# Kernel tuning notes

Hardware: AMD Instinct MI355X
Metric: run time of the kernel (lower is better)

Reference implementation:

```python
import jax, jax.numpy as jnp
import numpy as np

B, A, FEAT = 16, 256, 64
HID = 256
TEMB = 32
NUM_T = 100
L = 4
E = 131072
N = B * A


def _remove_mean(x):
    # x: [B, A, 3]
    return x - jnp.mean(x, axis=1, keepdims=True)


def setup_inputs() -> dict:
    key = jax.random.key(0)
    ks = jax.random.split(key, 24)
    s = 0.02
    inp = {
        "h": jax.random.normal(ks[0], (B, A, FEAT), jnp.float32),
        "x0": jax.random.normal(ks[1], (B, A, 3), jnp.float32),
        "noise": jax.random.normal(ks[2], (B, A, 3), jnp.float32),
        "t": jax.random.randint(ks[3], (B,), 0, NUM_T, jnp.int32),
        "row": jax.random.randint(ks[4], (E,), 0, N, jnp.int32),
        "col": jax.random.randint(ks[5], (E,), 0, N, jnp.int32),
        # node embedding
        "W_emb": jax.random.normal(ks[6], (FEAT + TEMB, HID), jnp.float32) * s,
        "b_emb": jnp.zeros((HID,), jnp.float32),
        # per-layer EGNN params, stacked over L layers
        "eW1": jax.random.normal(ks[7], (L, 2 * HID + 1, HID), jnp.float32) * s,
        "eb1": jnp.zeros((L, HID), jnp.float32),
        "eW2": jax.random.normal(ks[8], (L, HID, HID), jnp.float32) * s,
        "eb2": jnp.zeros((L, HID), jnp.float32),
        "cW1": jax.random.normal(ks[9], (L, HID, HID), jnp.float32) * s,
        "cb1": jnp.zeros((L, HID), jnp.float32),
        "cW2": jax.random.normal(ks[10], (L, HID, 1), jnp.float32) * s,
        "nW1": jax.random.normal(ks[11], (L, 2 * HID, HID), jnp.float32) * s,
        "nb1": jnp.zeros((L, HID), jnp.float32),
        "nW2": jax.random.normal(ks[12], (L, HID, HID), jnp.float32) * s,
        "nb2": jnp.zeros((L, HID), jnp.float32),
    }
    return inp


def _time_embedding(t):
    half = TEMB // 2
    freq = jnp.exp(jnp.arange(half, dtype=jnp.float32) * (-np.log(10000.0) / (half - 1)))
    ang = t.astype(jnp.float32)[:, None] * freq[None, :]  # [B, half]
    return jnp.concatenate([jnp.sin(ang), jnp.cos(ang)], axis=-1)  # [B, TEMB]


def _egnn_layer(h, x, row, col, eW1, eb1, eW2, eb2, cW1, cb1, cW2, nW1, nb1, nW2, nb2):
    coord_diff = x[row] - x[col]                                  # [E, 3]
    radial = jnp.sum(coord_diff * coord_diff, axis=1, keepdims=True)  # [E, 1]
    edge_in = jnp.concatenate([h[row], h[col], radial], axis=1)   # [E, 2H+1]
    m = jax.nn.silu(edge_in @ eW1 + eb1)
    m_ij = jax.nn.silu(m @ eW2 + eb2)                             # [E, H]
    w = jax.nn.silu(m_ij @ cW1 + cb1) @ cW2                       # [E, 1]
    coord_update = coord_diff * w                                 # [E, 3]
    x_new = x + jax.ops.segment_sum(coord_update, row, num_segments=N)
    m_i = jax.ops.segment_sum(m_ij, row, num_segments=N)          # [N, H]
    node_in = jnp.concatenate([h, m_i], axis=1)
    h_new = h + (jax.nn.silu(node_in @ nW1 + nb1) @ nW2 + nb2)
    return h_new, x_new


def reference(h, x0, noise, W_emb, b_emb, eW1, eb1, eW2, eb2, cW1, cb1, cW2,
              nW1, nb1, nW2, nb2, t, row, col):
    # diffusion schedule
    betas = jnp.linspace(1e-4, 0.02, NUM_T, dtype=jnp.float32)
    alphas_cumprod = jnp.cumprod(1.0 - betas)
    # forward diffusion q(x_t | x_0)
    noise = _remove_mean(noise)
    ab = alphas_cumprod[t][:, None, None]                          # [B,1,1]
    xt = jnp.sqrt(ab) * x0 + jnp.sqrt(1.0 - ab) * noise
    xt = _remove_mean(xt)

    t_emb = _time_embedding(t)                                     # [B, TEMB]
    t_emb_flat = jnp.repeat(t_emb, A, axis=0)                      # [N, TEMB]
    h_flat = h.reshape(N, FEAT)
    xt_flat = xt.reshape(N, 3)
    h_in = jnp.concatenate([h_flat, t_emb_flat], axis=-1)

    hh = h_in @ W_emb + b_emb                                      # [N, H]
    xx = xt_flat
    for l in range(L):
        hh, xx = _egnn_layer(hh, xx, row, col,
                             eW1[l], eb1[l], eW2[l], eb2[l],
                             cW1[l], cb1[l], cW2[l],
                             nW1[l], nb1[l], nW2[l], nb2[l])

    noise_pred = (xx - xt_flat).reshape(B, A, 3)
    noise_pred = _remove_mean(noise_pred)
    loss = jnp.mean((noise_pred - noise) ** 2)
    return loss
```

## Files before the change

### kernel.cpp

```cpp
#include <hip/hip_runtime.h>

#define NB 16
#define NA 256
#define NNODES 4096
#define FEATD 64
#define HID 256
#define TEMBD 32
#define NUMT 100
#define NE 131072
#define NL 4
#define NCHUNK (NE / 16)

typedef __attribute__((ext_vector_type(8))) short short8;
typedef __attribute__((ext_vector_type(4))) float f32x4;
typedef __attribute__((ext_vector_type(2))) float f32x2;

__device__ __forceinline__ float silu_f(float v) {
    float s = __builtin_amdgcn_rcpf(1.f + __builtin_amdgcn_exp2f(-1.44269504f * v));
    return v * s;
}

__device__ __forceinline__ short f2bf(float f) {
    union { float f; unsigned u; } v; v.f = f;
    unsigned r = (v.u + 0x7fffu + ((v.u >> 16) & 1u)) >> 16;
    return (short)r;
}
__device__ __forceinline__ short f2bf_t(float f) {
    union { float f; unsigned u; } v; v.f = f;
    return (short)(v.u >> 16);
}
__device__ __forceinline__ float bf2f(short s) {
    union { float f; unsigned u; } v; v.u = ((unsigned)(unsigned short)s) << 16;
    return v.f;
}

__device__ __forceinline__ float block_sum(float v, float* red, int a) {
    red[a] = v; __syncthreads();
    for (int s = 128; s > 0; s >>= 1) {
        if (a < s) red[a] += red[a + s];
        __syncthreads();
    }
    float r = red[0]; __syncthreads();
    return r;
}

__global__ __launch_bounds__(256) void prep_kernel(
    const float* __restrict__ x0, const float* __restrict__ noise,
    const int* __restrict__ t,
    float* __restrict__ noise_c, float* __restrict__ xt, float* __restrict__ temb,
    int* __restrict__ deg, float* __restrict__ out)
{
    __shared__ float red[256];
    __shared__ float sab_s[2];
    int b = blockIdx.x, a = threadIdx.x;
    int base = (b * NA + a) * 3;

    deg[b * 256 + a] = 0;
    if (b == 0 && a == 0) out[0] = 0.f;

    float nx = noise[base + 0], ny = noise[base + 1], nz = noise[base + 2];
    float mnx = block_sum(nx, red, a) * (1.f / NA);
    float mny = block_sum(ny, red, a) * (1.f / NA);
    float mnz = block_sum(nz, red, a) * (1.f / NA);
    nx -= mnx; ny -= mny; nz -= mnz;
    noise_c[base + 0] = nx; noise_c[base + 1] = ny; noise_c[base + 2] = nz;

    if (a == 0) {
        int tt = t[b];
        float p = 1.f;
        for (int i = 0; i < NUMT; i++) {
            float beta = 1e-4f + (0.02f - 1e-4f) * (float)i / (float)(NUMT - 1);
            if (i <= tt) p *= (1.f - beta);
        }
        sab_s[0] = sqrtf(p);
        sab_s[1] = sqrtf(1.f - p);
    }
    __syncthreads();
    float sab = sab_s[0], s1ab = sab_s[1];

    float xx = sab * x0[base + 0] + s1ab * nx;
    float xy = sab * x0[base + 1] + s1ab * ny;
    float xz = sab * x0[base + 2] + s1ab * nz;
    float mx = block_sum(xx, red, a) * (1.f / NA);
    float my = block_sum(xy, red, a) * (1.f / NA);
    float mz = block_sum(xz, red, a) * (1.f / NA);
    xt[base + 0] = xx - mx; xt[base + 1] = xy - my; xt[base + 2] = xz - mz;

    if (a < TEMBD / 2) {
        float fr = expf(-logf(10000.f) * (float)a / (float)(TEMBD / 2 - 1));
        float ang = (float)t[b] * fr;
        temb[b * TEMBD + a] = sinf(ang);
        temb[b * TEMBD + TEMBD / 2 + a] = cosf(ang);
    }
}

__global__ __launch_bounds__(256) void csr_hist(const int* __restrict__ row, int* __restrict__ deg)
{
    int i = blockIdx.x * 256 + threadIdx.x;
    if (i < NE) atomicAdd(&deg[row[i]], 1);
}

__global__ __launch_bounds__(256) void csr_scan(const int* __restrict__ deg, int* __restrict__ cursor)
{
    __shared__ int s[256];
    int t = threadIdx.x;
    int base = t * 16;
    int loc[16];
    int sum = 0;
    for (int i = 0; i < 16; i++) { loc[i] = sum; sum += deg[base + i]; }
    s[t] = sum; __syncthreads();
    for (int off = 1; off < 256; off <<= 1) {
        int v = (t >= off) ? s[t - off] : 0;
        __syncthreads();
        s[t] += v;
        __syncthreads();
    }
    int excl = (t == 0) ? 0 : s[t - 1];
    for (int i = 0; i < 16; i++) cursor[base + i] = excl + loc[i];
}

__global__ __launch_bounds__(256) void csr_scatter(
    const int* __restrict__ row, const int* __restrict__ col,
    int* __restrict__ cursor, int* __restrict__ prow, int* __restrict__ pcol)
{
    int i = blockIdx.x * 256 + threadIdx.x;
    if (i < NE) {
        int r = row[i];
        int p = atomicAdd(&cursor[r], 1);
        prow[p] = r;
        pcol[p] = col[i];
    }
}

__global__ __launch_bounds__(256) void csr_flag(
    const int* __restrict__ cursor, int* __restrict__ flag)
{
    int r = blockIdx.x * 256 + threadIdx.x;
    if (r >= NNODES) return;
    int end = cursor[r];
    int start = (r == 0) ? 0 : cursor[r - 1];
    int fl = 0;
    if (end > start) {
        int cs = start >> 4, ce = (end - 1) >> 4;
        for (int ch = cs; ch <= ce; ch++) {
            int rs = start > ch * 16 ? start : ch * 16;
            int re = end < ch * 16 + 16 ? end : ch * 16 + 16;
            if (rs > ch * 16 && re < ch * 16 + 16) fl = 1;
        }
    }
    flag[r] = fl;
}

#define WOFF_EMB 0
#define WOFF_L(l) (24576 + (l) * 458752)
#define WOFF_AB 0
#define WOFF_E2 131072
#define WOFF_C1 196608
#define WOFF_N1 262144
#define WOFF_N2 393216
#define W_TOTAL (24576 + 4 * 458752)

__global__ __launch_bounds__(256) void convert_weights(
    const float* __restrict__ W_emb, const float* __restrict__ eW1,
    const float* __restrict__ eW2, const float* __restrict__ cW1,
    const float* __restrict__ nW1, const float* __restrict__ nW2,
    short* __restrict__ wb)
{
    int idx = blockIdx.x * 256 + threadIdx.x;
    if (idx >= W_TOTAL) return;
    if (idx < 24576) {
        int k = idx >> 8, n = idx & 255;
        wb[WOFF_EMB + ((k >> 5) << 13) + (n << 5) + (k & 31)] = f2bf(W_emb[idx]);
        return;
    }
    int r = idx - 24576;
    int l = r / 458752;
    int o = r - l * 458752;
    if (o < 131072) {
        int k = o >> 9, n = o & 511;
        const float* src = eW1 + (size_t)l * 513 * 256 +
            (n < 256 ? (size_t)k * 256 + n : (size_t)(256 + k) * 256 + (n - 256));
        wb[WOFF_L(l) + WOFF_AB + ((k >> 5) * 16384) + (n << 5) + (k & 31)] = f2bf(*src);
        return;
    }
    const float* src; int dst; int o2;
    if (o < 196608)      { o2 = o - 131072; src = eW2 + (size_t)l * 65536 + o2;  dst = WOFF_L(l) + WOFF_E2; }
    else if (o < 262144) { o2 = o - 196608; src = cW1 + (size_t)l * 65536 + o2;  dst = WOFF_L(l) + WOFF_C1; }
    else if (o < 393216) { o2 = o - 262144; src = nW1 + (size_t)l * 131072 + o2; dst = WOFF_L(l) + WOFF_N1; }
    else                 { o2 = o - 393216; src = nW2 + (size_t)l * 65536 + o2;  dst = WOFF_L(l) + WOFF_N2; }
    int k = o2 >> 8, n = o2 & 255;
    wb[dst + ((k >> 5) << 13) + (n << 5) + (k & 31)] = f2bf(*src);
}

#define WF8_TOTAL (4 * 2 * 65536)
__global__ __launch_bounds__(256) void convert_weights_fp8(
    const float* __restrict__ eW2, const float* __restrict__ cW1,
    char* __restrict__ wf8)
{
    int idx = blockIdx.x * 256 + threadIdx.x;
    if (idx >= WF8_TOTAL) return;
    int l = idx >> 17;
    int o = idx & 131071;
    int mat = o >> 16;
    int o2 = o & 65535;
    int k = o2 >> 8, n = o2 & 255;
    const float* src = (mat == 0 ? eW2 : cW1) + (size_t)l * 65536 + (size_t)k * 256 + n;
    float v = (*src) * 16.f;
    int p = __builtin_amdgcn_cvt_pk_fp8_f32(v, v, 0, false);
    wf8[(size_t)l * 131072 + mat * 65536 + (k >> 5) * 8192 + n * 32 + (k & 31)] = (char)(p & 0xff);
}

__global__ __launch_bounds__(1024) void emb_p12_fused(
    const float* __restrict__ h, const float* __restrict__ temb,
    const short* __restrict__ wtEmb,
    const float* __restrict__ b_emb, const short* __restrict__ wtAB,
    const float* __restrict__ eb1_0,
    short* __restrict__ hh, short* __restrict__ P12)
{
    __shared__ short h2s[16 * 264];
    int tid = threadIdx.x;
    int wv = tid >> 6, l = tid & 63;
    int lr = l & 15, q = l >> 4;
    int r0 = blockIdx.x * 16;

    f32x4 acc = (f32x4){0.f, 0.f, 0.f, 0.f};
    int col0 = wv * 16 + lr;
    int n = r0 + lr;
    #pragma unroll
    for (int kt = 0; kt < 3; kt++) {
        int kk = kt * 32 + q * 8;
        const float* src = (kk < 64) ? &h[(size_t)n * 64 + kk]
                                     : &temb[(n >> 8) * 32 + kk - 64];
        short8 fa;
        #pragma unroll
        for (int k2 = 0; k2 < 8; k2++) fa[k2] = f2bf(src[k2]);
        short8 fb = *(const short8*)&wtEmb[kt * 8192 + col0 * 32 + q * 8];
        acc = __builtin_amdgcn_mfma_f32_16x16x32_bf16(fa, fb, acc, 0, 0, 0);
    }
    {
        float bv = b_emb[col0];
        #pragma unroll
        for (int rg = 0; rg < 4; rg++) {
            int rrow = q * 4 + rg;
            short b = f2bf(acc[rg] + bv);
            hh[(size_t)(r0 + rrow) * 256 + col0] = b;
            h2s[rrow * 264 + col0] = b;
        }
    }
    __syncthreads();

    f32x4 acc3[2];
    #pragma unroll
    for (int i = 0; i < 2; i++) acc3[i] = (f32x4){0.f, 0.f, 0.f, 0.f};
    #pragma unroll 2
    for (int kt = 0; kt < 8; kt++) {
        short8 fa = *(const short8*)&h2s[lr * 264 + kt * 32 + q * 8];
        #pragma unroll
        for (int nt = 0; nt < 2; nt++) {
            short8 fb = *(const short8*)&wtAB[kt * 16384 + (wv * 32 + nt * 16 + lr) * 32 + q * 8];
            acc3[nt] = __builtin_amdgcn_mfma_f32_16x16x32_bf16(fa, fb, acc3[nt], 0, 0, 0);
        }
    }
    #pragma unroll
    for (int nt = 0; nt < 2; nt++) {
        int col = wv * 32 + nt * 16 + lr;
        float bv = (col < 256) ? eb1_0[col] : 0.f;
        #pragma unroll
        for (int rg = 0; rg < 4; rg++)
            P12[(size_t)(r0 + q * 4 + rg) * 512 + col] = f2bf(acc3[nt][rg] + bv);
    }
}

__global__ __launch_bounds__(1024) void node_p12_fused(
    const short* __restrict__ hc, const float* __restrict__ m_i,
    const int* __restrict__ cursor, const int* __restrict__ flag,
    const int* __restrict__ tag0, const int* __restrict__ tag1,
    const float* __restrict__ msl0, const float* __restrict__ msl1,
    const float* __restrict__ xsl0, const float* __restrict__ xsl1,
    const float* __restrict__ x_agg, float* __restrict__ x_cur,
    const short* __restrict__ wtN1, const float* __restrict__ nb1,
    const short* __restrict__ wtN2, const float* __restrict__ nb2,
    const short* __restrict__ wtAB, const float* __restrict__ eb1n,
    short* __restrict__ hn, short* __restrict__ P12)
{
    __shared__ short m_is[16 * 264];
    __shared__ short t1s[16 * 264];
    __shared__ short h2s[16 * 264];
    int tid = threadIdx.x;
    int wv = tid >> 6, l = tid & 63;
    int lr = l & 15, q = l >> 4;
    int r0 = blockIdx.x * 16;

    {
        int rr = tid >> 6;
        int cc = (tid & 63) * 4;
        int r = r0 + rr;
        float v[4] = {0.f, 0.f, 0.f, 0.f};
        if (flag[r]) {
            float4 mv = *(const float4*)&m_i[(size_t)r * 256 + cc];
            v[0] = mv.x; v[1] = mv.y; v[2] = mv.z; v[3] = mv.w;
        }
        int end = cursor[r];
        int start = (r == 0) ? 0 : cursor[r - 1];
        if (end > start) {
            int cs = start >> 4, ce = (end - 1) >> 4;
            for (int ch = cs; ch <= ce; ch++) {
                if (tag0[ch] == r) {
                    float4 s0 = *(const float4*)&msl0[(size_t)ch * 256 + cc];
                    v[0] += s0.x; v[1] += s0.y; v[2] += s0.z; v[3] += s0.w;
                }
                if (tag1[ch] == r) {
                    float4 s1 = *(const float4*)&msl1[(size_t)ch * 256 + cc];
                    v[0] += s1.x; v[1] += s1.y; v[2] += s1.z; v[3] += s1.w;
                }
            }
        }
        #pragma unroll
        for (int i = 0; i < 4; i++) m_is[rr * 264 + cc + i] = f2bf(v[i]);
        if (tid < 16) {
            int r2 = r0 + tid;
            float sx = 0.f, sy = 0.f, sz = 0.f;
            if (flag[r2]) {
                sx = x_agg[r2 * 3 + 0]; sy = x_agg[r2 * 3 + 1]; sz = x_agg[r2 * 3 + 2];
            }
            int end2 = cursor[r2];
            int start2 = (r2 == 0) ? 0 : cursor[r2 - 1];
            if (end2 > start2) {
                int cs2 = start2 >> 4, ce2 = (end2 - 1) >> 4;
                for (int ch = cs2; ch <= ce2; ch++) {
                    if (tag0[ch] == r2) { sx += xsl0[ch * 3 + 0]; sy += xsl0[ch * 3 + 1]; sz += xsl0[ch * 3 + 2]; }
                    if (tag1[ch] == r2) { sx += xsl1[ch * 3 + 0]; sy += xsl1[ch * 3 + 1]; sz += xsl1[ch * 3 + 2]; }
                }
            }
            x_cur[r2 * 3 + 0] += sx;
            x_cur[r2 * 3 + 1] += sy;
            x_cur[r2 * 3 + 2] += sz;
        }
    }
    __syncthreads();

    int col0 = wv * 16 + lr;
    f32x4 acc = (f32x4){0.f, 0.f, 0.f, 0.f};
    #pragma unroll 2
    for (int kt = 0; kt < 16; kt++) {
        int kk = kt * 32 + q * 8;
        short8 fa;
        if (kk < 256) fa = *(const short8*)&hc[(size_t)(r0 + lr) * 256 + kk];
        else          fa = *(const short8*)&m_is[lr * 264 + kk - 256];
        short8 fb = *(const short8*)&wtN1[kt * 8192 + col0 * 32 + q * 8];
        acc = __builtin_amdgcn_mfma_f32_16x16x32_bf16(fa, fb, acc, 0, 0, 0);
    }
    {
        float bv = nb1[col0];
        #pragma unroll
        for (int rg = 0; rg < 4; rg++)
            t1s[(q * 4 + rg) * 264 + col0] = f2bf_t(silu_f(acc[rg] + bv));
    }
    __syncthreads();

    f32x4 acc2 = (f32x4){0.f, 0.f, 0.f, 0.f};
    #pragma unroll 2
    for (int kt = 0; kt < 8; kt++) {
        short8 fa = *(const short8*)&t1s[lr * 264 + kt * 32 + q * 8];
        short8 fb = *(const short8*)&wtN2[kt * 8192 + col0 * 32 + q * 8];
        acc2 = __builtin_amdgcn_mfma_f32_16x16x32_bf16(fa, fb, acc2, 0, 0, 0);
    }
    {
        float bv = nb2[col0];
        #pragma unroll
        for (int rg = 0; rg < 4; rg++) {
            int rrow = q * 4 + rg;
            float v = acc2[rg] + bv + bf2f(hc[(size_t)(r0 + rrow) * 256 + col0]);
            short b = f2bf(v);
            hn[(size_t)(r0 + rrow) * 256 + col0] = b;
            h2s[rrow * 264 + col0] = b;
        }
    }
    __syncthreads();

    f32x4 acc3[2];
    #pragma unroll
    for (int i = 0; i < 2; i++) acc3[i] = (f32x4){0.f, 0.f, 0.f, 0.f};
    #pragma unroll 2
    for (int kt = 0; kt < 8; kt++) {
        short8 fa = *(const short8*)&h2s[lr * 264 + kt * 32 + q * 8];
        #pragma unroll
        for (int nt = 0; nt < 2; nt++) {
            short8 fb = *(const short8*)&wtAB[kt * 16384 + (wv * 32 + nt * 16 + lr) * 32 + q * 8];
            acc3[nt] = __builtin_amdgcn_mfma_f32_16x16x32_bf16(fa, fb, acc3[nt], 0, 0, 0);
        }
    }
    #pragma unroll
    for (int nt = 0; nt < 2; nt++) {
        int col = wv * 32 + nt * 16 + lr;
        float bv = (col < 256) ? eb1n[col] : 0.f;
        #pragma unroll
        for (int rg = 0; rg < 4; rg++)
            P12[(size_t)(r0 + q * 4 + rg) * 512 + col] = f2bf(acc3[nt][rg] + bv);
    }
}

__global__ __launch_bounds__(256, 4) void egnn_edge_mfma(
    const short* __restrict__ P12, const float* __restrict__ x,
    const int* __restrict__ prow, const int* __restrict__ pcol,
    const float* __restrict__ w512,
    const char* __restrict__ wf8E2, const float* __restrict__ eb2,
    const char* __restrict__ wf8C1, const float* __restrict__ cb1,
    const float* __restrict__ cW2,
    float* __restrict__ m_i, float* __restrict__ x_agg,
    float* __restrict__ msl0, float* __restrict__ msl1,
    float* __restrict__ xsl0, float* __restrict__ xsl1,
    int* __restrict__ tag0, int* __restrict__ tag1, int do_mi)
{
    __shared__ __align__(16) char m_lds[64 * 272];
    __shared__ float cd_s[64][3];
    __shared__ int prow_s[64];
    __shared__ float wred[4][64];
    __shared__ float xtmp[64][3];

    int tid = threadIdx.x;
    int e0 = blockIdx.x * 64;
    int wv = tid >> 6, l = tid & 63;
    int lr = l & 15, q = l >> 4;

    {
        int e = tid >> 2, cq = tid & 3;
        int r = prow[e0 + e], c = pcol[e0 + e];
        float dx = x[r * 3 + 0] - x[c * 3 + 0];
        float dy = x[r * 3 + 1] - x[c * 3 + 1];
        float dz = x[r * 3 + 2] - x[c * 3 + 2];
        float rad = dx * dx + dy * dy + dz * dz;
        if (cq == 0) {
            prow_s[e] = r;
            cd_s[e][0] = dx; cd_s[e][1] = dy; cd_s[e][2] = dz;
        }
        const short* p1r = P12 + (size_t)r * 512;
        const short* p2r = P12 + (size_t)c * 512 + 256;
        #pragma unroll
        for (int j = 0; j < 8; j++) {
            int cb = (j >> 1) * 64 + (j & 1) * 32 + cq * 8;
            short8 a = *(const short8*)&p1r[cb];
            short8 b = *(const short8*)&p2r[cb];
            float4 w0 = *(const float4*)&w512[cb];
            float4 w1 = *(const float4*)&w512[cb + 4];
            float wv8[8] = {w0.x, w0.y, w0.z, w0.w, w1.x, w1.y, w1.z, w1.w};
            float s[8];
            #pragma unroll
            for (int k2 = 0; k2 < 8; k2++)
                s[k2] = silu_f(bf2f(a[k2]) + bf2f(b[k2]) + rad * wv8[k2]);
            int lo = __builtin_amdgcn_cvt_pk_fp8_f32(s[0], s[1], 0, false);
            lo = __builtin_amdgcn_cvt_pk_fp8_f32(s[2], s[3], lo, true);
            int hi = __builtin_amdgcn_cvt_pk_fp8_f32(s[4], s[5], 0, false);
            hi = __builtin_amdgcn_cvt_pk_fp8_f32(s[6], s[7], hi, true);
            int2 d = {lo, hi};
            *(int2*)&m_lds[e * 272 + cb] = d;
        }
    }
    __syncthreads();

    f32x4 acc[4][4];
    #pragma unroll
    for (int i = 0; i < 4; i++)
        #pragma unroll
        for (int j = 0; j < 4; j++) acc[i][j] = (f32x4){0.f, 0.f, 0.f, 0.f};
    #pragma unroll 2
    for (int kt = 0; kt < 8; kt++) {
        long fa[4], fb[4];
        #pragma unroll
        for (int mt = 0; mt < 4; mt++)
            fa[mt] = *(const long*)&m_lds[(mt * 16 + lr) * 272 + kt * 32 + q * 8];
        #pragma unroll
        for (int nt = 0; nt < 4; nt++)
            fb[nt] = *(const long*)&wf8E2[kt * 8192 + (wv * 64 + nt * 16 + lr) * 32 + q * 8];
        #pragma unroll
        for (int mt = 0; mt < 4; mt++)
            #pragma unroll
            for (int nt = 0; nt < 4; nt++)
                acc[mt][nt] = __builtin_amdgcn_mfma_f32_16x16x32_fp8_fp8(fa[mt], fb[nt], acc[mt][nt], 0, 0, 0);
    }
    __syncthreads();
    #pragma unroll
    for (int nt = 0; nt < 4; nt++) {
        int ccol = wv * 64 + nt * 16 + lr;
        float b2 = eb2[ccol];
        #pragma unroll
        for (int mt = 0; mt < 4; mt++)
            #pragma unroll
            for (int rg = 0; rg < 4; rg++) {
                int e = mt * 16 + q * 4 + rg;
                float v = silu_f(fmaf(acc[mt][nt][rg], 0.0625f, b2));
                int p = __builtin_amdgcn_cvt_pk_fp8_f32(v, v, 0, false);
                m_lds[e * 272 + ccol] = (char)(p & 0xff);
            }
    }
    __syncthreads();

    #pragma unroll
    for (int i = 0; i < 4; i++)
        #pragma unroll
        for (int j = 0; j < 4; j++) acc[i][j] = (f32x4){0.f, 0.f, 0.f, 0.f};
    #pragma unroll 2
    for (int kt = 0; kt < 8; kt++) {
        long fa[4], fb[4];
        #pragma unroll
        for (int mt = 0; mt < 4; mt++)
            fa[mt] = *(const long*)&m_lds[(mt * 16 + lr) * 272 + kt * 32 + q * 8];
        #pragma unroll
        for (int nt = 0; nt < 4; nt++)
            fb[nt] = *(const long*)&wf8C1[kt * 8192 + (wv * 64 + nt * 16 + lr) * 32 + q * 8];
        #pragma unroll
        for (int mt = 0; mt < 4; mt++)
            #pragma unroll
            for (int nt = 0; nt < 4; nt++)
                acc[mt][nt] = __builtin_amdgcn_mfma_f32_16x16x32_fp8_fp8(fa[mt], fb[nt], acc[mt][nt], 0, 0, 0);
    }

    if (do_mi) {
        int ebase = wv * 16;
        int c4 = l * 4;
        int chunk = blockIdx.x * 4 + wv;
        float a0 = 0.f, a1 = 0.f, a2 = 0.f, a3 = 0.f;
        int cur = prow_s[ebase];
        int nrun = 0;
        #pragma unroll
        for (int j = 0; j < 16; j++) {
            int e = ebase + j;
            int r = prow_s[e];
            if (r != cur) {
                float4 v = {a0, a1, a2, a3};
                if (nrun == 0) *(float4*)&msl0[(size_t)chunk * 256 + c4] = v;
                else           *(float4*)&m_i[(size_t)cur * 256 + c4] = v;
                nrun++; a0 = a1 = a2 = a3 = 0.f; cur = r;
            }
            int mv = *(const int*)&m_lds[e * 272 + c4];
            f32x2 lo = __builtin_amdgcn_cvt_pk_f32_fp8(mv, false);
            f32x2 hi = __builtin_amdgcn_cvt_pk_f32_fp8(mv, true);
            a0 += lo.x; a1 += lo.y; a2 += hi.x; a3 += hi.y;
        }
        float4 v = {a0, a1, a2, a3};
        if (nrun == 0) *(float4*)&msl0[(size_t)chunk * 256 + c4] = v;
        else           *(float4*)&msl1[(size_t)chunk * 256 + c4] = v;
        if (l == 0) {
            tag0[chunk] = prow_s[ebase];
            tag1[chunk] = nrun ? cur : -1;
        }
    }

    {
        float wp[4][4];
        #pragma unroll
        for (int i = 0; i < 4; i++)
            #pragma unroll
            for (int j = 0; j < 4; j++) wp[i][j] = 0.f;
        #pragma unroll
        for (int nt = 0; nt < 4; nt++) {
            int ccol = wv * 64 + nt * 16 + lr;
            float b1 = cb1[ccol];
            float c2 = cW2[ccol];
            #pragma unroll
            for (int mt = 0; mt < 4; mt++)
                #pragma unroll
                for (int rg = 0; rg < 4; rg++)
                    wp[mt][rg] += silu_f(fmaf(acc[mt][nt][rg], 0.0625f, b1)) * c2;
        }
        #pragma unroll
        for (int mt = 0; mt < 4; mt++)
            #pragma unroll
            for (int rg = 0; rg < 4; rg++) {
                float v = wp[mt][rg];
                v += __shfl_xor(v, 1, 64);
                v += __shfl_xor(v, 2, 64);
                v += __shfl_xor(v, 4, 64);
                v += __shfl_xor(v, 8, 64);
                if (lr == 0) wred[wv][mt * 16 + q * 4 + rg] = v;
            }
    }
    __syncthreads();
    if (tid < 64) {
        float w = wred[0][tid] + wred[1][tid] + wred[2][tid] + wred[3][tid];
        xtmp[tid][0] = cd_s[tid][0] * w;
        xtmp[tid][1] = cd_s[tid][1] * w;
        xtmp[tid][2] = cd_s[tid][2] * w;
    }
    __syncthreads();
    if (tid < 64) {
        int e = tid, j = e & 15, cw = e >> 4;
        int r = prow_s[e];
        bool leader = (j == 0) || (prow_s[e - 1] != r);
        if (leader) {
            int eend = (cw + 1) * 16;
            float sx = 0.f, sy = 0.f, sz = 0.f;
            int k = e;
            while (k < eend && prow_s[k] == r) {
                sx += xtmp[k][0]; sy += xtmp[k][1]; sz += xtmp[k][2]; k++;
            }
            int chunk = blockIdx.x * 4 + cw;
            if (j == 0)        { xsl0[chunk * 3 + 0] = sx; xsl0[chunk * 3 + 1] = sy; xsl0[chunk * 3 + 2] = sz; }
            else if (k == eend){ xsl1[chunk * 3 + 0] = sx; xsl1[chunk * 3 + 1] = sy; xsl1[chunk * 3 + 2] = sz; }
            else               { x_agg[r * 3 + 0] = sx; x_agg[r * 3 + 1] = sy; x_agg[r * 3 + 2] = sz; }
        }
    }
}

__global__ __launch_bounds__(256) void loss_part(
    const float* __restrict__ x_cur, const float* __restrict__ xt,
    const float* __restrict__ nc,
    const int* __restrict__ cursor, const int* __restrict__ flag,
    const int* __restrict__ tag0, const int* __restrict__ tag1,
    const float* __restrict__ xsl0, const float* __restrict__ xsl1,
    const float* __restrict__ x_agg,
    float* __restrict__ out)
{
    __shared__ float red[256];
    int b = blockIdx.x, a = threadIdx.x;
    int n = b * NA + a;
    int base = n * 3;

    float sx = 0.f, sy = 0.f, sz = 0.f;
    if (flag[n]) {
        sx = x_agg[base + 0]; sy = x_agg[base + 1]; sz = x_agg[base + 2];
    }
    int end = cursor[n];
    int start = (n == 0) ? 0 : cursor[n - 1];
    if (end > start) {
        int cs = start >> 4, ce = (end - 1) >> 4;
        for (int ch = cs; ch <= ce; ch++) {
            if (tag0[ch] == n) { sx += xsl0[ch * 3 + 0]; sy += xsl0[ch * 3 + 1]; sz += xsl0[ch * 3 + 2]; }
            if (tag1[ch] == n) { sx += xsl1[ch * 3 + 0]; sy += xsl1[ch * 3 + 1]; sz += xsl1[ch * 3 + 2]; }
        }
    }
    float px = x_cur[base + 0] + sx - xt[base + 0];
    float py = x_cur[base + 1] + sy - xt[base + 1];
    float pz = x_cur[base + 2] + sz - xt[base + 2];
    float mx = block_sum(px, red, a) * (1.f / NA);
    float my = block_sum(py, red, a) * (1.f / NA);
    float mz = block_sum(pz, red, a) * (1.f / NA);
    px -= mx; py -= my; pz -= mz;
    float dx = px - nc[base + 0], dy = py - nc[base + 1], dz = pz - nc[base + 2];
    float s = block_sum(dx * dx + dy * dy + dz * dz, red, a);
    if (a == 0) atomicAdd(out, s * (1.f / (float)(NNODES * 3)));
}

extern "C" void kernel_launch(void* const* d_in, const int* in_sizes, int n_in,
                              void* d_out, int out_size, void* d_ws, size_t ws_size,
                              hipStream_t stream)
{
    (void)in_sizes; (void)n_in; (void)out_size; (void)ws_size;
    const float* h     = (const float*)d_in[0];
    const float* x0    = (const float*)d_in[1];
    const float* noise = (const float*)d_in[2];
    const int*   t     = (const int*)d_in[3];
    const int*   row   = (const int*)d_in[4];
    const int*   col   = (const int*)d_in[5];
    const float* W_emb = (const float*)d_in[6];
    const float* b_emb = (const float*)d_in[7];
    const float* eW1   = (const float*)d_in[8];
    const float* eb1   = (const float*)d_in[9];
    const float* eW2   = (const float*)d_in[10];
    const float* eb2   = (const float*)d_in[11];
    const float* cW1   = (const float*)d_in[12];
    const float* cb1   = (const float*)d_in[13];
    const float* cW2   = (const float*)d_in[14];
    const float* nW1   = (const float*)d_in[15];
    const float* nb1   = (const float*)d_in[16];
    const float* nW2   = (const float*)d_in[17];
    const float* nb2   = (const float*)d_in[18];

    float* f = (float*)d_ws;
    size_t fo = 0;
    float* temb    = f + fo; fo += NB * TEMBD;
    float* noise_c = f + fo; fo += NNODES * 3;
    float* xt      = f + fo; fo += NNODES * 3;
    float* x_cur   = f + fo; fo += NNODES * 3;
    float* x_agg   = f + fo; fo += NNODES * 3;
    float* m_i     = f + fo; fo += (size_t)NNODES * HID;
    float* msl0    = f + fo; fo += (size_t)NCHUNK * 256;
    float* msl1    = f + fo; fo += (size_t)NCHUNK * 256;
    float* xsl0    = f + fo; fo += (size_t)NCHUNK * 3;
    float* xsl1    = f + fo; fo += (size_t)NCHUNK * 3;

    int* iw = (int*)(f + fo);
    size_t io = 0;
    int* deg    = iw + io; io += NNODES;
    int* cursor = iw + io; io += NNODES;
    int* flag   = iw + io; io += NNODES;
    int* prow   = iw + io; io += NE;
    int* pcol   = iw + io; io += NE;
    int* tag0   = iw + io; io += NCHUNK;
    int* tag1   = iw + io; io += NCHUNK;

    size_t sbase_bytes = ((((char*)(iw + io)) - (char*)d_ws) + 15) & ~(size_t)15;
    short* sb = (short*)((char*)d_ws + sbase_bytes);
    short* wb  = sb;
    size_t so = W_TOTAL;
    short* hh  = sb + so; so += (size_t)NNODES * HID;
    short* hh2 = sb + so; so += (size_t)NNODES * HID;
    short* P12 = sb + so; so += (size_t)NNODES * 512;
    char* wf8 = (char*)(sb + so);

    prep_kernel<<<NB, 256, 0, stream>>>(x0, noise, t, noise_c, xt, temb, deg, (float*)d_out);
    csr_hist<<<NE / 256, 256, 0, stream>>>(row, deg);
    csr_scan<<<1, 256, 0, stream>>>(deg, cursor);
    csr_scatter<<<NE / 256, 256, 0, stream>>>(row, col, cursor, prow, pcol);
    csr_flag<<<NNODES / 256, 256, 0, stream>>>(cursor, flag);
    convert_weights<<<(W_TOTAL + 255) / 256, 256, 0, stream>>>(W_emb, eW1, eW2, cW1, nW1, nW2, wb);
    convert_weights_fp8<<<WF8_TOTAL / 256, 256, 0, stream>>>(eW2, cW1, wf8);
    emb_p12_fused<<<NNODES / 16, 1024, 0, stream>>>(
        h, temb, wb + WOFF_EMB, b_emb, wb + WOFF_L(0) + WOFF_AB, eb1, hh, P12);
    hipMemcpyAsync(x_cur, xt, (size_t)NNODES * 3 * sizeof(float), hipMemcpyDeviceToDevice, stream);

    short* hc = hh;
    short* hn = hh2;
    for (int l = 0; l < NL; l++) {
        const short* wl = wb + WOFF_L(l);
        const char* wf8l = wf8 + (size_t)l * 131072;
        int last = (l == NL - 1);
        egnn_edge_mfma<<<NE / 64, 256, 0, stream>>>(
            P12, x_cur, prow, pcol,
            eW1 + (size_t)l * 513 * 256 + 512 * 256,
            wf8l, eb2 + (size_t)l * HID,
            wf8l + 65536, cb1 + (size_t)l * HID,
            cW2 + (size_t)l * HID,
            m_i, x_agg, msl0, msl1, xsl0, xsl1, tag0, tag1, last ? 0 : 1);
        if (!last) {
            node_p12_fused<<<NNODES / 16, 1024, 0, stream>>>(
                hc, m_i, cursor, flag, tag0, tag1, msl0, msl1,
                xsl0, xsl1, x_agg, x_cur,
                wl + WOFF_N1, nb1 + (size_t)l * HID,
                wl + WOFF_N2, nb2 + (size_t)l * HID,
                wb + WOFF_L(l + 1) + WOFF_AB, eb1 + (size_t)(l + 1) * HID,
                hn, P12);
            short* tmp = hc; hc = hn; hn = tmp;
        }
    }

    loss_part<<<NB, 256, 0, stream>>>(
        x_cur, xt, noise_c, cursor, flag, tag0, tag1, xsl0, xsl1, x_agg, (float*)d_out);
}
```

Measured before the change: 440.5 us.

## Fold small setup kernels together and retile node GEMMs to eight-row blocks

Three small launches disappear: the per-node flag computation moves into the CSR scan kernel, the fp8 weight conversion merges into the bf16 weight conversion, and the prep kernel writes x_cur directly instead of a device-to-device copy. The embedding and node-update fused kernels now use 8-row blocks of 512 threads, each wave covering more output columns. This doubles the grid for better CU coverage, but half of each 16-row MFMA tile holds duplicated rows, so matrix work per useful row doubles.

After: 468.3 us. 1.06x slower.

```diff
diff --git a/kernel.cpp b/kernel.cpp
--- a/kernel.cpp
+++ b/kernel.cpp
@@ -48,7 +48,7 @@
     const float* __restrict__ x0, const float* __restrict__ noise,
     const int* __restrict__ t,
     float* __restrict__ noise_c, float* __restrict__ xt, float* __restrict__ temb,
-    int* __restrict__ deg, float* __restrict__ out)
+    int* __restrict__ deg, float* __restrict__ out, float* __restrict__ x_cur)
 {
     __shared__ float red[256];
     __shared__ float sab_s[2];
@@ -84,7 +84,9 @@
     float mx = block_sum(xx, red, a) * (1.f / NA);
     float my = block_sum(xy, red, a) * (1.f / NA);
     float mz = block_sum(xz, red, a) * (1.f / NA);
-    xt[base + 0] = xx - mx; xt[base + 1] = xy - my; xt[base + 2] = xz - mz;
+    float vx = xx - mx, vy = xy - my, vz = xz - mz;
+    xt[base + 0] = vx; xt[base + 1] = vy; xt[base + 2] = vz;
+    x_cur[base + 0] = vx; x_cur[base + 1] = vy; x_cur[base + 2] = vz;
 
     if (a < TEMBD / 2) {
         float fr = expf(-logf(10000.f) * (float)a / (float)(TEMBD / 2 - 1));
@@ -100,14 +102,15 @@
     if (i < NE) atomicAdd(&deg[row[i]], 1);
 }
 
-__global__ __launch_bounds__(256) void csr_scan(const int* __restrict__ deg, int* __restrict__ cursor)
+__global__ __launch_bounds__(256) void csr_scan(
+    const int* __restrict__ deg, int* __restrict__ cursor, int* __restrict__ flag)
 {
     __shared__ int s[256];
     int t = threadIdx.x;
     int base = t * 16;
-    int loc[16];
+    int loc[16], dg[16];
     int sum = 0;
-    for (int i = 0; i < 16; i++) { loc[i] = sum; sum += deg[base + i]; }
+    for (int i = 0; i < 16; i++) { dg[i] = deg[base + i]; loc[i] = sum; sum += dg[i]; }
     s[t] = sum; __syncthreads();
     for (int off = 1; off < 256; off <<= 1) {
         int v = (t >= off) ? s[t - off] : 0;
@@ -116,7 +119,21 @@
         __syncthreads();
     }
     int excl = (t == 0) ? 0 : s[t - 1];
-    for (int i = 0; i < 16; i++) cursor[base + i] = excl + loc[i];
+    for (int i = 0; i < 16; i++) {
+        int start = excl + loc[i];
+        cursor[base + i] = start;
+        int end = start + dg[i];
+        int fl = 0;
+        if (end > start) {
+            int cs = start >> 4, ce = (end - 1) >> 4;
+            for (int ch = cs; ch <= ce; ch++) {
+                int rs = start > ch * 16 ? start : ch * 16;
+                int re = end < ch * 16 + 16 ? end : ch * 16 + 16;
+                if (rs > ch * 16 && re < ch * 16 + 16) fl = 1;
+            }
+        }
+        flag[base + i] = fl;
+    }
 }
 
 __global__ __launch_bounds__(256) void csr_scatter(
@@ -130,25 +147,6 @@
         prow[p] = r;
         pcol[p] = col[i];
     }
-}
-
-__global__ __launch_bounds__(256) void csr_flag(
-    const int* __restrict__ cursor, int* __restrict__ flag)
-{
-    int r = blockIdx.x * 256 + threadIdx.x;
-    if (r >= NNODES) return;
-    int end = cursor[r];
-    int start = (r == 0) ? 0 : cursor[r - 1];
-    int fl = 0;
-    if (end > start) {
-        int cs = start >> 4, ce = (end - 1) >> 4;
-        for (int ch = cs; ch <= ce; ch++) {
-            int rs = start > ch * 16 ? start : ch * 16;
-            int re = end < ch * 16 + 16 ? end : ch * 16 + 16;
-            if (rs > ch * 16 && re < ch * 16 + 16) fl = 1;
-        }
-    }
-    flag[r] = fl;
 }
 
 #define WOFF_EMB 0
@@ -159,15 +157,29 @@
 #define WOFF_N1 262144
 #define WOFF_N2 393216
 #define W_TOTAL (24576 + 4 * 458752)
+#define WF8_TOTAL (4 * 2 * 65536)
 
 __global__ __launch_bounds__(256) void convert_weights(
     const float* __restrict__ W_emb, const float* __restrict__ eW1,
     const float* __restrict__ eW2, const float* __restrict__ cW1,
     const float* __restrict__ nW1, const float* __restrict__ nW2,
-    short* __restrict__ wb)
+    short* __restrict__ wb, char* __restrict__ wf8)
 {
     int idx = blockIdx.x * 256 + threadIdx.x;
-    if (idx >= W_TOTAL) return;
+    if (idx >= W_TOTAL) {
+        int i8 = idx - W_TOTAL;
+        if (i8 >= WF8_TOTAL) return;
+        int l = i8 >> 17;
+        int o = i8 & 131071;
+        int mat = o >> 16;
+        int o2 = o & 65535;
+        int k = o2 >> 8, n = o2 & 255;
+        const float* src = (mat == 0 ? eW2 : cW1) + (size_t)l * 65536 + (size_t)k * 256 + n;
+        float v = (*src) * 16.f;
+        int p = __builtin_amdgcn_cvt_pk_fp8_f32(v, v, 0, false);
+        wf8[(size_t)l * 131072 + mat * 65536 + (k >> 5) * 8192 + n * 32 + (k & 31)] = (char)(p & 0xff);
+        return;
+    }
     if (idx < 24576) {
         int k = idx >> 8, n = idx & 255;
         wb[WOFF_EMB + ((k >> 5) << 13) + (n << 5) + (k & 31)] = f2bf(W_emb[idx]);
@@ -192,40 +204,24 @@
     wb[dst + ((k >> 5) << 13) + (n << 5) + (k & 31)] = f2bf(*src);
 }
 
-#define WF8_TOTAL (4 * 2 * 65536)
-__global__ __launch_bounds__(256) void convert_weights_fp8(
-    const float* __restrict__ eW2, const float* __restrict__ cW1,
-    char* __restrict__ wf8)
-{
-    int idx = blockIdx.x * 256 + threadIdx.x;
-    if (idx >= WF8_TOTAL) return;
-    int l = idx >> 17;
-    int o = idx & 131071;
-    int mat = o >> 16;
-    int o2 = o & 65535;
-    int k = o2 >> 8, n = o2 & 255;
-    const float* src = (mat == 0 ? eW2 : cW1) + (size_t)l * 65536 + (size_t)k * 256 + n;
-    float v = (*src) * 16.f;
-    int p = __builtin_amdgcn_cvt_pk_fp8_f32(v, v, 0, false);
-    wf8[(size_t)l * 131072 + mat * 65536 + (k >> 5) * 8192 + n * 32 + (k & 31)] = (char)(p & 0xff);
-}
-
-__global__ __launch_bounds__(1024) void emb_p12_fused(
+__global__ __launch_bounds__(512, 4) void emb_p12_fused(
     const float* __restrict__ h, const float* __restrict__ temb,
     const short* __restrict__ wtEmb,
     const float* __restrict__ b_emb, const short* __restrict__ wtAB,
     const float* __restrict__ eb1_0,
     short* __restrict__ hh, short* __restrict__ P12)
 {
-    __shared__ short h2s[16 * 264];
+    __shared__ short h2s[8 * 264];
     int tid = threadIdx.x;
     int wv = tid >> 6, l = tid & 63;
     int lr = l & 15, q = l >> 4;
-    int r0 = blockIdx.x * 16;
-
-    f32x4 acc = (f32x4){0.f, 0.f, 0.f, 0.f};
-    int col0 = wv * 16 + lr;
-    int n = r0 + lr;
+    int alr = lr & 7;
+    int r0 = blockIdx.x * 8;
+
+    f32x4 acc[2];
+    #pragma unroll
+    for (int i = 0; i < 2; i++) acc[i] = (f32x4){0.f, 0.f, 0.f, 0.f};
+    int n = r0 + alr;
     #pragma unroll
     for (int kt = 0; kt < 3; kt++) {
         int kk = kt * 32 + q * 8;
@@ -234,44 +230,53 @@
         short8 fa;
         #pragma unroll
         for (int k2 = 0; k2 < 8; k2++) fa[k2] = f2bf(src[k2]);
-        short8 fb = *(const short8*)&wtEmb[kt * 8192 + col0 * 32 + q * 8];
-        acc = __builtin_amdgcn_mfma_f32_16x16x32_bf16(fa, fb, acc, 0, 0, 0);
-    }
-    {
-        float bv = b_emb[col0];
-        #pragma unroll
-        for (int rg = 0; rg < 4; rg++) {
-            int rrow = q * 4 + rg;
-            short b = f2bf(acc[rg] + bv);
-            hh[(size_t)(r0 + rrow) * 256 + col0] = b;
-            h2s[rrow * 264 + col0] = b;
-        }
-    }
-    __syncthreads();
-
-    f32x4 acc3[2];
-    #pragma unroll
-    for (int i = 0; i < 2; i++) acc3[i] = (f32x4){0.f, 0.f, 0.f, 0.f};
+        #pragma unroll
+        for (int nt = 0; nt < 2; nt++) {
+            short8 fb = *(const short8*)&wtEmb[kt * 8192 + (wv * 32 + nt * 16 + lr) * 32 + q * 8];
+            acc[nt] = __builtin_amdgcn_mfma_f32_16x16x32_bf16(fa, fb, acc[nt], 0, 0, 0);
+        }
+    }
+    if (q < 2) {
+        #pragma unroll
+        for (int nt = 0; nt < 2; nt++) {
+            int col = wv * 32 + nt * 16 + lr;
+            float bv = b_emb[col];
+            #pragma unroll
+            for (int rg = 0; rg < 4; rg++) {
+                int rrow = q * 4 + rg;
+                short b = f2bf(acc[nt][rg] + bv);
+                hh[(size_t)(r0 + rrow) * 256 + col] = b;
+                h2s[rrow * 264 + col] = b;
+            }
+        }
+    }
+    __syncthreads();
+
+    f32x4 acc3[4];
+    #pragma unroll
+    for (int i = 0; i < 4; i++) acc3[i] = (f32x4){0.f, 0.f, 0.f, 0.f};
     #pragma unroll 2
     for (int kt = 0; kt < 8; kt++) {
-        short8 fa = *(const short8*)&h2s[lr * 264 + kt * 32 + q * 8];
-        #pragma unroll
-        for (int nt = 0; nt < 2; nt++) {
-            short8 fb = *(const short8*)&wtAB[kt * 16384 + (wv * 32 + nt * 16 + lr) * 32 + q * 8];
+        short8 fa = *(const short8*)&h2s[alr * 264 + kt * 32 + q * 8];
+        #pragma unroll
+        for (int nt = 0; nt < 4; nt++) {
+            short8 fb = *(const short8*)&wtAB[kt * 16384 + (wv * 64 + nt * 16 + lr) * 32 + q * 8];
             acc3[nt] = __builtin_amdgcn_mfma_f32_16x16x32_bf16(fa, fb, acc3[nt], 0, 0, 0);
         }
     }
-    #pragma unroll
-    for (int nt = 0; nt < 2; nt++) {
-        int col = wv * 32 + nt * 16 + lr;
-        float bv = (col < 256) ? eb1_0[col] : 0.f;
-        #pragma unroll
-        for (int rg = 0; rg < 4; rg++)
-            P12[(size_t)(r0 + q * 4 + rg) * 512 + col] = f2bf(acc3[nt][rg] + bv);
-    }
-}
-
-__global__ __launch_bounds__(1024) void node_p12_fused(
+    if (q < 2) {
+        #pragma unroll
+        for (int nt = 0; nt < 4; nt++) {
+            int col = wv * 64 + nt * 16 + lr;
+            float bv = (col < 256) ? eb1_0[col] : 0.f;
+            #pragma unroll
+            for (int rg = 0; rg < 4; rg++)
+                P12[(size_t)(r0 + q * 4 + rg) * 512 + col] = f2bf(acc3[nt][rg] + bv);
+        }
+    }
+}
+
+__global__ __launch_bounds__(512, 4) void node_p12_fused(
     const short* __restrict__ hc, const float* __restrict__ m_i,
     const int* __restrict__ cursor, const int* __restrict__ flag,
     const int* __restrict__ tag0, const int* __restrict__ tag1,
@@ -283,13 +288,14 @@
     const short* __restrict__ wtAB, const float* __restrict__ eb1n,
     short* __restrict__ hn, short* __restrict__ P12)
 {
-    __shared__ short m_is[16 * 264];
-    __shared__ short t1s[16 * 264];
-    __shared__ short h2s[16 * 264];
+    __shared__ short m_is[8 * 264];
+    __shared__ short t1s[8 * 264];
+    __shared__ short h2s[8 * 264];
     int tid = threadIdx.x;
     int wv = tid >> 6, l = tid & 63;
     int lr = l & 15, q = l >> 4;
-    int r0 = blockIdx.x * 16;
+    int alr = lr & 7;
+    int r0 = blockIdx.x * 8;
 
     {
         int rr = tid >> 6;
@@ -317,7 +323,7 @@
         }
         #pragma unroll
         for (int i = 0; i < 4; i++) m_is[rr * 264 + cc + i] = f2bf(v[i]);
-        if (tid < 16) {
+        if (tid < 8) {
             int r2 = r0 + tid;
             float sx = 0.f, sy = 0.f, sz = 0.f;
             if (flag[r2]) {
@@ -339,64 +345,83 @@
     }
     __syncthreads();
 
-    int col0 = wv * 16 + lr;
-    f32x4 acc = (f32x4){0.f, 0.f, 0.f, 0.f};
+    f32x4 acc[2];
+    #pragma unroll
+    for (int i = 0; i < 2; i++) acc[i] = (f32x4){0.f, 0.f, 0.f, 0.f};
     #pragma unroll 2
     for (int kt = 0; kt < 16; kt++) {
         int kk = kt * 32 + q * 8;
         short8 fa;
-        if (kk < 256) fa = *(const short8*)&hc[(size_t)(r0 + lr) * 256 + kk];
-        else          fa = *(const short8*)&m_is[lr * 264 + kk - 256];
-        short8 fb = *(const short8*)&wtN1[kt * 8192 + col0 * 32 + q * 8];
-        acc = __builtin_amdgcn_mfma_f32_16x16x32_bf16(fa, fb, acc, 0, 0, 0);
-    }
-    {
-        float bv = nb1[col0];
-        #pragma unroll
-        for (int rg = 0; rg < 4; rg++)
-            t1s[(q * 4 + rg) * 264 + col0] = f2bf_t(silu_f(acc[rg] + bv));
-    }
-    __syncthreads();
-
-    f32x4 acc2 = (f32x4){0.f, 0.f, 0.f, 0.f};
+        if (kk < 256) fa = *(const short8*)&hc[(size_t)(r0 + alr) * 256 + kk];
+        else          fa = *(const short8*)&m_is[alr * 264 + kk - 256];
+        #pragma unroll
+        for (int nt = 0; nt < 2; nt++) {
+            short8 fb = *(const short8*)&wtN1[kt * 8192 + (wv * 32 + nt * 16 + lr) * 32 + q * 8];
+            acc[nt] = __builtin_amdgcn_mfma_f32_16x16x32_bf16(fa, fb, acc[nt], 0, 0, 0);
+        }
+    }
+    if (q < 2) {
+        #pragma unroll
+        for (int nt = 0; nt < 2; nt++) {
+            int col = wv * 32 + nt * 16 + lr;
+            float bv = nb1[col];
+            #pragma unroll
+            for (int rg = 0; rg < 4; rg++)
+                t1s[(q * 4 + rg) * 264 + col] = f2bf_t(silu_f(acc[nt][rg] + bv));
+        }
+    }
+    __syncthreads();
+
+    f32x4 acc2[2];
+    #pragma unroll
+    for (int i = 0; i < 2; i++) acc2[i] = (f32x4){0.f, 0.f, 0.f, 0.f};
     #pragma unroll 2
     for (int kt = 0; kt < 8; kt++) {
-        short8 fa = *(const short8*)&t1s[lr * 264 + kt * 32 + q * 8];
-        short8 fb = *(const short8*)&wtN2[kt * 8192 + col0 * 32 + q * 8];
-        acc2 = __builtin_amdgcn_mfma_f32_16x16x32_bf16(fa, fb, acc2, 0, 0, 0);
-    }
-    {
-        float bv = nb2[col0];
-        #pragma unroll
-        for (int rg = 0; rg < 4; rg++) {
-            int rrow = q * 4 + rg;
-            float v = acc2[rg] + bv + bf2f(hc[(size_t)(r0 + rrow) * 256 + col0]);
-            short b = f2bf(v);
-            hn[(size_t)(r0 + rrow) * 256 + col0] = b;
-            h2s[rrow * 264 + col0] = b;
-        }
-    }
-    __syncthreads();
-
-    f32x4 acc3[2];
-    #pragma unroll
-    for (int i = 0; i < 2; i++) acc3[i] = (f32x4){0.f, 0.f, 0.f, 0.f};
+        short8 fa = *(const short8*)&t1s[alr * 264 + kt * 32 + q * 8];
+        #pragma unroll
+        for (int nt = 0; nt < 2; nt++) {
+            short8 fb = *(const short8*)&wtN2[kt * 8192 + (wv * 32 + nt * 16 + lr) * 32 + q * 8];
+            acc2[nt] = __builtin_amdgcn_mfma_f32_16x16x32_bf16(fa, fb, acc2[nt], 0, 0, 0);
+        }
+    }
+    if (q < 2) {
+        #pragma unroll
+        for (int nt = 0; nt < 2; nt++) {
+            int col = wv * 32 + nt * 16 + lr;
+            float bv = nb2[col];
+            #pragma unroll
+            for (int rg = 0; rg < 4; rg++) {
+                int rrow = q * 4 + rg;
+                float v = acc2[nt][rg] + bv + bf2f(hc[(size_t)(r0 + rrow) * 256 + col]);
+                short b = f2bf(v);
+                hn[(size_t)(r0 + rrow) * 256 + col] = b;
+                h2s[rrow * 264 + col] = b;
+            }
+        }
+    }
+    __syncthreads();
+
+    f32x4 acc3[4];
+    #pragma unroll
+    for (int i = 0; i < 4; i++) acc3[i] = (f32x4){0.f, 0.f, 0.f, 0.f};
     #pragma unroll 2
     for (int kt = 0; kt < 8; kt++) {
-        short8 fa = *(const short8*)&h2s[lr * 264 + kt * 32 + q * 8];
-        #pragma unroll
-        for (int nt = 0; nt < 2; nt++) {
-            short8 fb = *(const short8*)&wtAB[kt * 16384 + (wv * 32 + nt * 16 + lr) * 32 + q * 8];
+        short8 fa = *(const short8*)&h2s[alr * 264 + kt * 32 + q * 8];
+        #pragma unroll
+        for (int nt = 0; nt < 4; nt++) {
+            short8 fb = *(const short8*)&wtAB[kt * 16384 + (wv * 64 + nt * 16 + lr) * 32 + q * 8];
             acc3[nt] = __builtin_amdgcn_mfma_f32_16x16x32_bf16(fa, fb, acc3[nt], 0, 0, 0);
         }
     }
-    #pragma unroll
-    for (int nt = 0; nt < 2; nt++) {
-        int col = wv * 32 + nt * 16 + lr;
-        float bv = (col < 256) ? eb1n[col] : 0.f;
-        #pragma unroll
-        for (int rg = 0; rg < 4; rg++)
-            P12[(size_t)(r0 + q * 4 + rg) * 512 + col] = f2bf(acc3[nt][rg] + bv);
+    if (q < 2) {
+        #pragma unroll
+        for (int nt = 0; nt < 4; nt++) {
+            int col = wv * 64 + nt * 16 + lr;
+            float bv = (col < 256) ? eb1n[col] : 0.f;
+            #pragma unroll
+            for (int rg = 0; rg < 4; rg++)
+                P12[(size_t)(r0 + q * 4 + rg) * 512 + col] = f2bf(acc3[nt][rg] + bv);
+        }
     }
 }
 
@@ -698,16 +723,14 @@
     short* P12 = sb + so; so += (size_t)NNODES * 512;
     char* wf8 = (char*)(sb + so);
 
-    prep_kernel<<<NB, 256, 0, stream>>>(x0, noise, t, noise_c, xt, temb, deg, (float*)d_out);
+    prep_kernel<<<NB, 256, 0, stream>>>(x0, noise, t, noise_c, xt, temb, deg, (float*)d_out, x_cur);
     csr_hist<<<NE / 256, 256, 0, stream>>>(row, deg);
-    csr_scan<<<1, 256, 0, stream>>>(deg, cursor);
+    csr_scan<<<1, 256, 0, stream>>>(deg, cursor, flag);
     csr_scatter<<<NE / 256, 256, 0, stream>>>(row, col, cursor, prow, pcol);
-    csr_flag<<<NNODES / 256, 256, 0, stream>>>(cursor, flag);
-    convert_weights<<<(W_TOTAL + 255) / 256, 256, 0, stream>>>(W_emb, eW1, eW2, cW1, nW1, nW2, wb);
-    convert_weights_fp8<<<WF8_TOTAL / 256, 256, 0, stream>>>(eW2, cW1, wf8);
-    emb_p12_fused<<<NNODES / 16, 1024, 0, stream>>>(
+    convert_weights<<<(W_TOTAL + WF8_TOTAL + 255) / 256, 256, 0, stream>>>(
+        W_emb, eW1, eW2, cW1, nW1, nW2, wb, wf8);
+    emb_p12_fused<<<NNODES / 8, 512, 0, stream>>>(
         h, temb, wb + WOFF_EMB, b_emb, wb + WOFF_L(0) + WOFF_AB, eb1, hh, P12);
-    hipMemcpyAsync(x_cur, xt, (size_t)NNODES * 3 * sizeof(float), hipMemcpyDeviceToDevice, stream);
 
     short* hc = hh;
     short* hn = hh2;
@@ -723,7 +746,7 @@
             cW2 + (size_t)l * HID,
             m_i, x_agg, msl0, msl1, xsl0, xsl1, tag0, tag1, last ? 0 : 1);
         if (!last) {
-            node_p12_fused<<<NNODES / 16, 1024, 0, stream>>>(
+            node_p12_fused<<<NNODES / 8, 512, 0, stream>>>(
                 hc, m_i, cursor, flag, tag0, tag1, msl0, msl1,
                 xsl0, xsl1, x_agg, x_cur,
                 wl + WOFF_N1, nb1 + (size_t)l * HID,
```
